# Optimization experiments

Measured on AMD Instinct MI355X. Metric: run time of the kernel, lower is better.

## Reference

```python
import jax, jax.numpy as jnp
import numpy as np

N_HEADS = 32
N_KV_HEADS = 8
HEAD_DIM = 128
DIM = 4096
ROPE_THETA = 500000.0
B, S = 2, 2048


def setup_inputs() -> dict:
    key = jax.random.key(0)
    k1, k2, k3, k4, k5 = jax.random.split(key, 5)
    sd = 0.02
    return {
        "x": jax.random.normal(k1, (B, S, DIM), dtype=jnp.float32),
        "wq": jax.random.normal(k2, (DIM, N_HEADS * HEAD_DIM), dtype=jnp.float32) * sd,
        "wk": jax.random.normal(k3, (DIM, N_KV_HEADS * HEAD_DIM), dtype=jnp.float32) * sd,
        "wv": jax.random.normal(k4, (DIM, N_KV_HEADS * HEAD_DIM), dtype=jnp.float32) * sd,
        "wo": jax.random.normal(k5, (N_HEADS * HEAD_DIM, DIM), dtype=jnp.float32) * sd,
    }


def _rope_freqs(seqlen, head_dim, theta):
    inv = 1.0 / (theta ** (jnp.arange(0, head_dim, 2, dtype=jnp.float32) / head_dim))
    ang = jnp.arange(seqlen, dtype=jnp.float32)[:, None] * inv[None, :]  # [S, hd/2]
    return jnp.cos(ang), jnp.sin(ang)


def _apply_rope(t, cos, sin):
    # t: [B, S, H, hd]; complex multiply on interleaved (even, odd) pairs
    tr = t.reshape(*t.shape[:-1], HEAD_DIM // 2, 2)
    a, b = tr[..., 0], tr[..., 1]
    c = cos[None, :, None, :]
    s = sin[None, :, None, :]
    out = jnp.stack([a * c - b * s, a * s + b * c], axis=-1)
    return out.reshape(t.shape)


def reference(x, wq, wk, wv, wo):
    bsz, seqlen, _ = x.shape
    n_rep = N_HEADS // N_KV_HEADS
    q = (x @ wq).reshape(bsz, seqlen, N_HEADS, HEAD_DIM)
    k = (x @ wk).reshape(bsz, seqlen, N_KV_HEADS, HEAD_DIM)
    v = (x @ wv).reshape(bsz, seqlen, N_KV_HEADS, HEAD_DIM)

    cos, sin = _rope_freqs(seqlen, HEAD_DIM, ROPE_THETA)
    q = _apply_rope(q, cos, sin)
    k = _apply_rope(k, cos, sin)

    # repeat_kv: expand kv heads to n_heads (torch.repeat_interleave dim=2)
    k = jnp.repeat(k, n_rep, axis=2)  # [B, S, H, hd]
    v = jnp.repeat(v, n_rep, axis=2)

    scale = 1.0 / jnp.sqrt(jnp.float32(HEAD_DIM))
    scores = jnp.einsum("bqhd,bkhd->bhqk", q, k) * scale  # [B, H, S, S]
    causal = jnp.tril(jnp.ones((seqlen, seqlen), dtype=bool))
    scores = jnp.where(causal[None, None], scores, jnp.float32(-1e9))
    probs = jax.nn.softmax(scores, axis=-1)
    out = jnp.einsum("bhqk,bkhd->bqhd", probs, v)  # [B, S, H, hd]
    out = out.reshape(bsz, seqlen, N_HEADS * HEAD_DIM)
    return out @ wo
```

## Files before the change

### kernel.cpp

```cpp
#include <hip/hip_runtime.h>
#include <stdint.h>

typedef unsigned short u16;
using short8 = __attribute__((ext_vector_type(8))) short;
using f32x4  = __attribute__((ext_vector_type(4))) float;

#define S_LEN 2048
#define NH 32
#define NKV 8
#define HD 128
#define DIM 4096
#define NQ 4096
#define NKVD 1024

typedef __attribute__((address_space(1))) unsigned int uGLB;
typedef __attribute__((address_space(3))) unsigned int uLDS;

__device__ __forceinline__ void g2l16(const u16* g, u16* l) {
  __builtin_amdgcn_global_load_lds((const uGLB*)g, (uLDS*)l, 16, 0, 0);
}

__device__ __forceinline__ float b2f(u16 u) {
  union { unsigned u32; float f; } x; x.u32 = ((unsigned)u) << 16; return x.f;
}
__device__ __forceinline__ u16 f2b(float f) {
  union { float f; unsigned u32; } x; x.f = f;
  unsigned lsb = (x.u32 >> 16) & 1u;
  x.u32 += 0x7fffu + lsb;
  return (u16)(x.u32 >> 16);
}

__global__ __launch_bounds__(256) void transpose_cast(const float* __restrict__ in,
                                                      u16* __restrict__ out,
                                                      int K, int N) {
  __shared__ float tile[32][33];
  int n0 = blockIdx.x * 32, k0 = blockIdx.y * 32;
  int tx = threadIdx.x, ty = threadIdx.y;
#pragma unroll
  for (int j = 0; j < 4; ++j)
    tile[ty + j * 8][tx] = in[(size_t)(k0 + ty + j * 8) * N + n0 + tx];
  __syncthreads();
#pragma unroll
  for (int j = 0; j < 4; ++j)
    out[(size_t)(n0 + ty + j * 8) * K + k0 + tx] = f2b(tile[tx][ty + j * 8]);
}

__global__ __launch_bounds__(256) void cast_x(const float* __restrict__ in,
                                              u16* __restrict__ out, int n4) {
  int i = blockIdx.x * 256 + threadIdx.x;
  if (i >= n4) return;
  float4 v = reinterpret_cast<const float4*>(in)[i];
  ushort4 u;
  u.x = f2b(v.x); u.y = f2b(v.y); u.z = f2b(v.z); u.w = f2b(v.w);
  reinterpret_cast<ushort4*>(out)[i] = u;
}

__global__ __launch_bounds__(512) void gemm256(const u16* __restrict__ A,
                                               const u16* __restrict__ Bt,
                                               int N,
                                               float* __restrict__ out) {
  const int K = 4096;
  const int NT = 64;
  __shared__ __align__(16) u16 lds[2][2][2][8192];

  int tid  = threadIdx.x;
  int lane = tid & 63, w = tid >> 6;
  int ml   = lane & 15, quad = lane >> 4;
  int wm   = w >> 2, wn = w & 3;

  int bid = blockIdx.y * gridDim.x + blockIdx.x;
  int xcd = bid & 7, idx = bid >> 3;
  int bx = (xcd & 3) * 4 + (idx & 3);
  int by = (xcd >> 2) * 8 + (idx >> 2);
  int m0 = by * 256, n0 = bx * 256;

  int dstB = w * 1024 + lane * 16;
  int r    = dstB >> 7;
  int cg   = ((dstB >> 4) & 7) ^ (r & 7);
  const u16* pA = A  + (size_t)(m0 + r) * K + cg * 8;
  const u16* pB = Bt + (size_t)(n0 + r) * K + cg * 8;

#define STAGE(mat, T, hh) do { \
    int _b = (T) & 1; \
    int _Tc = (T) < NT ? (T) : (NT - 1); \
    const u16* _s = ((mat) ? pB : pA) + (size_t)(hh) * 128 * K + (size_t)_Tc * 64; \
    u16* _d = &lds[_b][mat][hh][w * 512]; \
    g2l16(_s, _d); \
    g2l16(_s + (size_t)64 * K, _d + 4096); \
  } while (0)

  f32x4 acc[8][4] = {};
  int cxa  = (quad ^ (ml & 7)) << 4;
  int aoff = ml * 128 + cxa;
  int boff = (wn & 1) * 8192 + aoff;

  STAGE(0, 0, 0); STAGE(0, 0, 1); STAGE(1, 0, 0); STAGE(1, 0, 1);
  STAGE(0, 1, 0);
  asm volatile("s_waitcnt vmcnt(2)" ::: "memory");
  __builtin_amdgcn_s_barrier();

  short8 af[4][2], bf0[2][2], bf1[2][2];

  for (int t = 0; t < NT; ++t) {
    int buf = t & 1;
    const char* Ab = reinterpret_cast<const char*>(&lds[buf][0][wm][0]);
    const char* Bb = reinterpret_cast<const char*>(&lds[buf][1][wn >> 1][0]);

#pragma unroll
    for (int mi = 0; mi < 4; ++mi)
#pragma unroll
      for (int ks = 0; ks < 2; ++ks)
        af[mi][ks] = *reinterpret_cast<const short8*>(Ab + (aoff ^ (ks << 6)) + mi * 2048);
#pragma unroll
    for (int ni = 0; ni < 2; ++ni)
#pragma unroll
      for (int ks = 0; ks < 2; ++ks)
        bf0[ni][ks] = *reinterpret_cast<const short8*>(Bb + (boff ^ (ks << 6)) + ni * 2048);
    STAGE(0, t + 1, 1);
    __builtin_amdgcn_s_barrier();
    asm volatile("s_waitcnt lgkmcnt(0)" ::: "memory");
    __builtin_amdgcn_sched_barrier(0);
    __builtin_amdgcn_s_setprio(1);
#pragma unroll
    for (int mi = 0; mi < 4; ++mi)
#pragma unroll
      for (int ni = 0; ni < 2; ++ni)
#pragma unroll
        for (int ks = 0; ks < 2; ++ks)
          acc[mi][ni] = __builtin_amdgcn_mfma_f32_16x16x32_bf16(af[mi][ks], bf0[ni][ks], acc[mi][ni], 0, 0, 0);
    __builtin_amdgcn_s_setprio(0);
    __builtin_amdgcn_s_barrier();

#pragma unroll
    for (int ni = 0; ni < 2; ++ni)
#pragma unroll
      for (int ks = 0; ks < 2; ++ks)
        bf1[ni][ks] = *reinterpret_cast<const short8*>(Bb + (boff ^ (ks << 6)) + (2 + ni) * 2048);
    STAGE(1, t + 1, 0);
    __builtin_amdgcn_s_barrier();
    asm volatile("s_waitcnt lgkmcnt(0)" ::: "memory");
    __builtin_amdgcn_sched_barrier(0);
    __builtin_amdgcn_s_setprio(1);
#pragma unroll
    for (int mi = 0; mi < 4; ++mi)
#pragma unroll
      for (int ni = 0; ni < 2; ++ni)
#pragma unroll
        for (int ks = 0; ks < 2; ++ks)
          acc[mi][2 + ni] = __builtin_amdgcn_mfma_f32_16x16x32_bf16(af[mi][ks], bf1[ni][ks], acc[mi][2 + ni], 0, 0, 0);
    __builtin_amdgcn_s_setprio(0);
    __builtin_amdgcn_s_barrier();

#pragma unroll
    for (int mi = 0; mi < 4; ++mi)
#pragma unroll
      for (int ks = 0; ks < 2; ++ks)
        af[mi][ks] = *reinterpret_cast<const short8*>(Ab + 8192 + (aoff ^ (ks << 6)) + mi * 2048);
    STAGE(1, t + 1, 1);
    __builtin_amdgcn_s_barrier();
    asm volatile("s_waitcnt lgkmcnt(0)" ::: "memory");
    __builtin_amdgcn_sched_barrier(0);
    __builtin_amdgcn_s_setprio(1);
#pragma unroll
    for (int mi = 0; mi < 4; ++mi)
#pragma unroll
      for (int ni = 0; ni < 2; ++ni)
#pragma unroll
        for (int ks = 0; ks < 2; ++ks)
          acc[4 + mi][ni] = __builtin_amdgcn_mfma_f32_16x16x32_bf16(af[mi][ks], bf0[ni][ks], acc[4 + mi][ni], 0, 0, 0);
    __builtin_amdgcn_s_setprio(0);
    __builtin_amdgcn_s_barrier();

    STAGE(0, t + 2, 0);
    __builtin_amdgcn_s_barrier();
    __builtin_amdgcn_s_setprio(1);
#pragma unroll
    for (int mi = 0; mi < 4; ++mi)
#pragma unroll
      for (int ni = 0; ni < 2; ++ni)
#pragma unroll
        for (int ks = 0; ks < 2; ++ks)
          acc[4 + mi][2 + ni] = __builtin_amdgcn_mfma_f32_16x16x32_bf16(af[mi][ks], bf1[ni][ks], acc[4 + mi][2 + ni], 0, 0, 0);
    __builtin_amdgcn_s_setprio(0);
    asm volatile("s_waitcnt vmcnt(2)" ::: "memory");
    __builtin_amdgcn_s_barrier();
  }
#undef STAGE

#pragma unroll
  for (int mi = 0; mi < 8; ++mi) {
#pragma unroll
    for (int ni = 0; ni < 4; ++ni) {
#pragma unroll
      for (int rr = 0; rr < 4; ++rr) {
        int row = m0 + wm * 128 + mi * 16 + quad * 4 + rr;
        int col = n0 + wn * 64 + ni * 16 + ml;
        out[(size_t)row * N + col] = acc[mi][ni][rr];
      }
    }
  }
}

__global__ __launch_bounds__(512) void gemm128(const u16* __restrict__ A,
                                               const u16* __restrict__ Bt,
                                               u16* __restrict__ Qb,
                                               u16* __restrict__ Kb,
                                               u16* __restrict__ Vt) {
  const int K = 4096;
  const int NT = 64;
  __shared__ __align__(16) char L[98304];

  int tid  = threadIdx.x;
  int lane = tid & 63, w = tid >> 6;
  int ml   = lane & 15, quad = lane >> 4;
  int wm   = w >> 2, wn = w & 3;

  int bid = blockIdx.y * gridDim.x + blockIdx.x;
  int xcd = bid & 7, idx = bid >> 3;
  int bx = (xcd & 3) * 6 + idx % 6;
  int by = (xcd >> 2) * 16 + idx / 6;
  int m0 = by * 128, n0 = bx * 256;

  int dstB = w * 1024 + lane * 16;
  int r    = dstB >> 7;
  int cg   = ((dstB >> 4) & 7) ^ (r & 7);
  const u16* pA = A  + (size_t)(m0 + r) * K + cg * 8;
  const u16* pB = Bt + (size_t)(n0 + r) * K + cg * 8;

#define STAGE_A(T, h) do { \
    int _b = (T) & 1; int _Tc = (T) < NT ? (T) : (NT - 1); \
    g2l16(pA + (size_t)(h) * 64 * K + (size_t)_Tc * 64, \
          (u16*)(L + _b * 16384 + (h) * 8192 + w * 1024)); \
  } while (0)
#define STAGE_B(T, h) do { \
    int _b = (T) & 1; int _Tc = (T) < NT ? (T) : (NT - 1); \
    const u16* _s = pB + (size_t)(h) * 128 * K + (size_t)_Tc * 64; \
    char* _d = L + 32768 + _b * 32768 + (h) * 16384 + w * 1024; \
    g2l16(_s, (u16*)_d); \
    g2l16(_s + (size_t)64 * K, (u16*)(_d + 8192)); \
  } while (0)

  f32x4 acc[4][4] = {};
  int cxa  = (quad ^ (ml & 7)) << 4;
  int aoff = ml * 128 + cxa;
  int boff = (wn & 1) * 8192 + aoff;

  STAGE_A(0, 0); STAGE_A(0, 1); STAGE_B(0, 0); STAGE_B(0, 1);
  STAGE_B(1, 0); STAGE_B(1, 1);
  asm volatile("s_waitcnt vmcnt(4)" ::: "memory");
  __builtin_amdgcn_s_barrier();

  short8 af[2][2], af2[2][2], bf[4][2];

  for (int t = 0; t < NT; ++t) {
    int buf = t & 1;
    const char* Ab = L + buf * 16384 + wm * 8192;
    const char* Bb = L + 32768 + buf * 32768 + (wn >> 1) * 16384;

#pragma unroll
    for (int mi = 0; mi < 2; ++mi)
#pragma unroll
      for (int ks = 0; ks < 2; ++ks)
        af[mi][ks] = *reinterpret_cast<const short8*>(Ab + (aoff ^ (ks << 6)) + mi * 2048);
#pragma unroll
    for (int ni = 0; ni < 4; ++ni)
#pragma unroll
      for (int ks = 0; ks < 2; ++ks)
        bf[ni][ks] = *reinterpret_cast<const short8*>(Bb + (boff ^ (ks << 6)) + ni * 2048);
    STAGE_A(t + 1, 0); STAGE_A(t + 1, 1);
    __builtin_amdgcn_s_barrier();
    asm volatile("s_waitcnt lgkmcnt(0)" ::: "memory");
    __builtin_amdgcn_sched_barrier(0);
    __builtin_amdgcn_s_setprio(1);
#pragma unroll
    for (int mi = 0; mi < 2; ++mi)
#pragma unroll
      for (int ni = 0; ni < 4; ++ni)
#pragma unroll
        for (int ks = 0; ks < 2; ++ks)
          acc[mi][ni] = __builtin_amdgcn_mfma_f32_16x16x32_bf16(af[mi][ks], bf[ni][ks], acc[mi][ni], 0, 0, 0);
    __builtin_amdgcn_s_setprio(0);
    __builtin_amdgcn_s_barrier();

#pragma unroll
    for (int mi = 0; mi < 2; ++mi)
#pragma unroll
      for (int ks = 0; ks < 2; ++ks)
        af2[mi][ks] = *reinterpret_cast<const short8*>(Ab + 4096 + (aoff ^ (ks << 6)) + mi * 2048);
    STAGE_B(t + 2, 0); STAGE_B(t + 2, 1);
    __builtin_amdgcn_s_barrier();
    asm volatile("s_waitcnt lgkmcnt(0)" ::: "memory");
    __builtin_amdgcn_sched_barrier(0);
    __builtin_amdgcn_s_setprio(1);
#pragma unroll
    for (int mi = 0; mi < 2; ++mi)
#pragma unroll
      for (int ni = 0; ni < 4; ++ni)
#pragma unroll
        for (int ks = 0; ks < 2; ++ks)
          acc[2 + mi][ni] = __builtin_amdgcn_mfma_f32_16x16x32_bf16(af2[mi][ks], bf[ni][ks], acc[2 + mi][ni], 0, 0, 0);
    __builtin_amdgcn_s_setprio(0);
    asm volatile("s_waitcnt vmcnt(4)" ::: "memory");
    __builtin_amdgcn_s_barrier();
  }
#undef STAGE_A
#undef STAGE_B

#pragma unroll
  for (int a = 0; a < 4; ++a) {
#pragma unroll
    for (int ni = 0; ni < 4; ++ni) {
#pragma unroll
      for (int rr = 0; rr < 4; ++rr) {
        int row = m0 + wm * 64 + a * 16 + quad * 4 + rr;
        int col = n0 + wn * 64 + ni * 16 + ml;
        float v = acc[a][ni][rr];
        int b = row >> 11, s = row & (S_LEN - 1);
        if (col < NQ) {
          int h = col >> 7, d = col & 127;
          Qb[((size_t)((b * NH + h) * S_LEN + s)) * HD + d] = f2b(v);
        } else if (col < NQ + NKVD) {
          int cc = col - NQ; int h = cc >> 7, d = cc & 127;
          Kb[((size_t)((b * NKV + h) * S_LEN + s)) * HD + d] = f2b(v);
        } else {
          int cc = col - NQ - NKVD; int h = cc >> 7, d = cc & 127;
          Vt[((size_t)((b * NKV + h) * HD + d)) * S_LEN + s] = f2b(v);
        }
      }
    }
  }
}

__global__ __launch_bounds__(256) void rope_ip(u16* __restrict__ X, int npairs) {
  int idx = blockIdx.x * 256 + threadIdx.x;
  if (idx >= npairs) return;
  int i = idx & 63;
  int s = (idx >> 6) & (S_LEN - 1);
  float inv = __expf(-0.2050369278939421f * (float)i);
  float ang = (float)s * inv;
  float sn, cs;
  sincosf(ang, &sn, &cs);
  ushort2 pr = reinterpret_cast<ushort2*>(X)[idx];
  float a = b2f(pr.x), b = b2f(pr.y);
  ushort2 o;
  o.x = f2b(a * cs - b * sn);
  o.y = f2b(a * sn + b * cs);
  reinterpret_cast<ushort2*>(X)[idx] = o;
}

__global__ __launch_bounds__(256, 3) void flash(const u16* __restrict__ Qb,
                                                const u16* __restrict__ Kb,
                                                const u16* __restrict__ Vt,
                                                u16* __restrict__ AO) {
  __shared__ __align__(16) u16 Ks[64 * 128];
  __shared__ __align__(16) u16 Vs[128 * 64];
  __shared__ __align__(16) u16 Ps[4 * 16 * 80];

  int tid  = threadIdx.x;
  int lane = tid & 63, w = tid >> 6;
  int ml   = lane & 15, quad = lane >> 4;
  int q_tile = blockIdx.x, h = blockIdx.y, b = blockIdx.z;
  int hkv = h >> 2;
  int q0  = q_tile * 64;
  const u16* Qh = Qb + ((size_t)(b * NH + h) * S_LEN) * HD;
  const u16* Kh = Kb + ((size_t)(b * NKV + hkv) * S_LEN) * HD;
  const u16* Vh = Vt + ((size_t)(b * NKV + hkv) * HD) * S_LEN;
  u16* Pw = Ps + w * 16 * 80;

  short8 qf[4];
#pragma unroll
  for (int ks = 0; ks < 4; ++ks)
    qf[ks] = *reinterpret_cast<const short8*>(
        Qh + (size_t)(q0 + w * 16 + ml) * HD + ks * 32 + quad * 8);

  short8 ones8;
  {
    u16 one_b = 0x3f80;
#pragma unroll
    for (int j = 0; j < 8; ++j) ones8[j] = (short)one_b;
  }

  f32x4 o[8] = {};
  f32x4 o9 = {};
  const float SC = 0.12751745f;
  const float BIAS = 18.0f;

  int qg = q0 + w * 16 + ml;
  int ntile = q_tile + 1;
  for (int it = 0; it < ntile; ++it) {
    int kv0 = it * 64;
    __syncthreads();
#pragma unroll
    for (int p = 0; p < 4; ++p) {
      int slot = w * 256 + p * 64 + lane;
      int krow = slot >> 4, kch = slot & 15;
      int ksrc = kch ^ (krow & 15);
      g2l16(Kh + (size_t)(kv0 + krow) * HD + ksrc * 8, &Ks[(w * 256 + p * 64) * 8]);
      int vrow = slot >> 3, vch = slot & 7;
      int vsrc = vch ^ (vrow & 7);
      g2l16(Vh + (size_t)vrow * S_LEN + kv0 + vsrc * 8, &Vs[(w * 256 + p * 64) * 8]);
    }
    __syncthreads();

    f32x4 st[4] = {};
#pragma unroll
    for (int ks = 0; ks < 4; ++ks) {
#pragma unroll
      for (int nt = 0; nt < 4; ++nt) {
        int row = nt * 16 + ml;
        int ch = ((ks << 2) | quad) ^ ml;
        short8 kf = *reinterpret_cast<const short8*>(&Ks[row * 128 + ch * 8]);
        st[nt] = __builtin_amdgcn_mfma_f32_16x16x32_bf16(kf, qf[ks], st[nt], 0, 0, 0);
      }
    }

    bool diag = (it == q_tile);
#pragma unroll
    for (int nt = 0; nt < 4; ++nt) {
      float p0 = exp2f(fmaf(st[nt][0], SC, -BIAS));
      float p1 = exp2f(fmaf(st[nt][1], SC, -BIAS));
      float p2 = exp2f(fmaf(st[nt][2], SC, -BIAS));
      float p3 = exp2f(fmaf(st[nt][3], SC, -BIAS));
      if (diag) {
        int kg = kv0 + nt * 16 + quad * 4;
        if (kg + 0 > qg) p0 = 0.f;
        if (kg + 1 > qg) p1 = 0.f;
        if (kg + 2 > qg) p2 = 0.f;
        if (kg + 3 > qg) p3 = 0.f;
      }
      uint2 pk;
      pk.x = (unsigned)f2b(p0) | ((unsigned)f2b(p1) << 16);
      pk.y = (unsigned)f2b(p2) | ((unsigned)f2b(p3) << 16);
      *reinterpret_cast<uint2*>(&Pw[ml * 80 + nt * 16 + quad * 4]) = pk;
    }

#pragma unroll
    for (int ks2 = 0; ks2 < 2; ++ks2) {
      short8 pf = *reinterpret_cast<const short8*>(&Pw[ml * 80 + ks2 * 32 + quad * 8]);
#pragma unroll
      for (int dt = 0; dt < 8; ++dt) {
        int row = dt * 16 + ml;
        int ch = ((ks2 << 2) | quad) ^ (ml & 7);
        short8 vf = *reinterpret_cast<const short8*>(&Vs[row * 64 + ch * 8]);
        o[dt] = __builtin_amdgcn_mfma_f32_16x16x32_bf16(pf, vf, o[dt], 0, 0, 0);
      }
      o9 = __builtin_amdgcn_mfma_f32_16x16x32_bf16(pf, ones8, o9, 0, 0, 0);
    }
  }

  size_t row_base = (size_t)(b * S_LEN + q0 + w * 16 + quad * 4);
#pragma unroll
  for (int rr = 0; rr < 4; ++rr) {
    float inv_l = 1.0f / o9[rr];
#pragma unroll
    for (int dt = 0; dt < 8; ++dt) {
      int col = h * HD + dt * 16 + ml;
      AO[(row_base + rr) * (size_t)DIM + col] = f2b(o[dt][rr] * inv_l);
    }
  }
}

extern "C" void kernel_launch(void* const* d_in, const int* in_sizes, int n_in,
                              void* d_out, int out_size, void* d_ws, size_t ws_size,
                              hipStream_t stream) {
  const float* x  = (const float*)d_in[0];
  const float* wq = (const float*)d_in[1];
  const float* wk = (const float*)d_in[2];
  const float* wv = (const float*)d_in[3];
  const float* wo = (const float*)d_in[4];
  float* out = (float*)d_out;
  char* ws = (char*)d_ws;

  u16* Wqt = (u16*)(ws + 0);
  u16* Wkt = (u16*)(ws + 33554432);
  u16* Wvt = (u16*)(ws + 41943040);
  u16* Xb  = (u16*)(ws + 50331648);
  u16* Qb  = (u16*)(ws + 83886080);
  u16* Kb  = (u16*)(ws + 117440512);
  u16* Vt  = (u16*)(ws + 125829120);

  transpose_cast<<<dim3(128, 128), dim3(32, 8), 0, stream>>>(wq, Wqt, 4096, 4096);
  transpose_cast<<<dim3(32, 128),  dim3(32, 8), 0, stream>>>(wk, Wkt, 4096, 1024);
  transpose_cast<<<dim3(32, 128),  dim3(32, 8), 0, stream>>>(wv, Wvt, 4096, 1024);
  cast_x<<<16384, 256, 0, stream>>>(x, Xb, 4194304);

  gemm128<<<dim3(24, 32), 512, 0, stream>>>(Xb, Wqt, Qb, Kb, Vt);

  rope_ip<<<32768, 256, 0, stream>>>(Qb, 8388608);
  rope_ip<<<8192, 256, 0, stream>>>(Kb, 2097152);

  transpose_cast<<<dim3(128, 128), dim3(32, 8), 0, stream>>>(wo, Wqt, 4096, 4096);

  flash<<<dim3(32, 32, 2), 256, 0, stream>>>(Qb, Kb, Vt, Xb);

  gemm256<<<dim3(16, 16), 512, 0, stream>>>(Xb, Wqt, 4096, out);
}
```

Before: 806.1 us.

## Double-buffer K/V tiles in flash attention and schedule heavy query tiles first

Double-buffers the K and V LDS tiles so the async global-to-LDS load of the next KV tile is issued before computing on the current one. Explicit vmcnt waits and barriers replace the two __syncthreads per iteration. It also reverses the query-tile order so the longest causal blocks launch first, and pads the P scratch row stride from 80 to 88 to reduce bank conflicts. The doubled LDS footprint lowers the occupancy hint from 3 to 2 blocks per CU, giving up some latency hiding from concurrent blocks.

```diff
diff --git a/kernel.cpp b/kernel.cpp
--- a/kernel.cpp
+++ b/kernel.cpp
@@ -348,24 +348,25 @@
   reinterpret_cast<ushort2*>(X)[idx] = o;
 }
 
-__global__ __launch_bounds__(256, 3) void flash(const u16* __restrict__ Qb,
+__global__ __launch_bounds__(256, 2) void flash(const u16* __restrict__ Qb,
                                                 const u16* __restrict__ Kb,
                                                 const u16* __restrict__ Vt,
                                                 u16* __restrict__ AO) {
-  __shared__ __align__(16) u16 Ks[64 * 128];
-  __shared__ __align__(16) u16 Vs[128 * 64];
-  __shared__ __align__(16) u16 Ps[4 * 16 * 80];
+  __shared__ __align__(16) u16 Ks[2][64 * 128];
+  __shared__ __align__(16) u16 Vs[2][128 * 64];
+  __shared__ __align__(16) u16 Ps[4 * 16 * 88];
 
   int tid  = threadIdx.x;
   int lane = tid & 63, w = tid >> 6;
   int ml   = lane & 15, quad = lane >> 4;
-  int q_tile = blockIdx.x, h = blockIdx.y, b = blockIdx.z;
+  int q_tile = gridDim.x - 1 - blockIdx.x;
+  int h = blockIdx.y, b = blockIdx.z;
   int hkv = h >> 2;
   int q0  = q_tile * 64;
   const u16* Qh = Qb + ((size_t)(b * NH + h) * S_LEN) * HD;
   const u16* Kh = Kb + ((size_t)(b * NKV + hkv) * S_LEN) * HD;
   const u16* Vh = Vt + ((size_t)(b * NKV + hkv) * HD) * S_LEN;
-  u16* Pw = Ps + w * 16 * 80;
+  u16* Pw = Ps + w * 16 * 88;
 
   short8 qf[4];
 #pragma unroll
@@ -385,22 +386,39 @@
   const float SC = 0.12751745f;
   const float BIAS = 18.0f;
 
+#define STAGE_KV(IT, D) do { \
+    int _kv0 = (IT) * 64; \
+    _Pragma("unroll") \
+    for (int p = 0; p < 4; ++p) { \
+      int slot = w * 256 + p * 64 + lane; \
+      int krow = slot >> 4, kch = slot & 15; \
+      int ksrc = kch ^ (krow & 15); \
+      g2l16(Kh + (size_t)(_kv0 + krow) * HD + ksrc * 8, &Ks[D][(w * 256 + p * 64) * 8]); \
+      int vrow = slot >> 3, vch = slot & 7; \
+      int vsrc = vch ^ (vrow & 7); \
+      g2l16(Vh + (size_t)vrow * S_LEN + _kv0 + vsrc * 8, &Vs[D][(w * 256 + p * 64) * 8]); \
+    } \
+  } while (0)
+
   int qg = q0 + w * 16 + ml;
   int ntile = q_tile + 1;
+
+  STAGE_KV(0, 0);
+
   for (int it = 0; it < ntile; ++it) {
+    int cur = it & 1;
+    if (it + 1 < ntile) {
+      STAGE_KV(it + 1, cur ^ 1);
+      asm volatile("s_waitcnt vmcnt(8)" ::: "memory");
+    } else {
+      asm volatile("s_waitcnt vmcnt(0)" ::: "memory");
+    }
+    __builtin_amdgcn_s_barrier();
+    __builtin_amdgcn_sched_barrier(0);
+
     int kv0 = it * 64;
-    __syncthreads();
-#pragma unroll
-    for (int p = 0; p < 4; ++p) {
-      int slot = w * 256 + p * 64 + lane;
-      int krow = slot >> 4, kch = slot & 15;
-      int ksrc = kch ^ (krow & 15);
-      g2l16(Kh + (size_t)(kv0 + krow) * HD + ksrc * 8, &Ks[(w * 256 + p * 64) * 8]);
-      int vrow = slot >> 3, vch = slot & 7;
-      int vsrc = vch ^ (vrow & 7);
-      g2l16(Vh + (size_t)vrow * S_LEN + kv0 + vsrc * 8, &Vs[(w * 256 + p * 64) * 8]);
-    }
-    __syncthreads();
+    const u16* Kc = &Ks[cur][0];
+    const u16* Vc = &Vs[cur][0];
 
     f32x4 st[4] = {};
 #pragma unroll
@@ -409,7 +427,7 @@
       for (int nt = 0; nt < 4; ++nt) {
         int row = nt * 16 + ml;
         int ch = ((ks << 2) | quad) ^ ml;
-        short8 kf = *reinterpret_cast<const short8*>(&Ks[row * 128 + ch * 8]);
+        short8 kf = *reinterpret_cast<const short8*>(&Kc[row * 128 + ch * 8]);
         st[nt] = __builtin_amdgcn_mfma_f32_16x16x32_bf16(kf, qf[ks], st[nt], 0, 0, 0);
       }
     }
@@ -431,22 +449,26 @@
       uint2 pk;
       pk.x = (unsigned)f2b(p0) | ((unsigned)f2b(p1) << 16);
       pk.y = (unsigned)f2b(p2) | ((unsigned)f2b(p3) << 16);
-      *reinterpret_cast<uint2*>(&Pw[ml * 80 + nt * 16 + quad * 4]) = pk;
+      *reinterpret_cast<uint2*>(&Pw[ml * 88 + nt * 16 + quad * 4]) = pk;
     }
 
 #pragma unroll
     for (int ks2 = 0; ks2 < 2; ++ks2) {
-      short8 pf = *reinterpret_cast<const short8*>(&Pw[ml * 80 + ks2 * 32 + quad * 8]);
+      short8 pf = *reinterpret_cast<const short8*>(&Pw[ml * 88 + ks2 * 32 + quad * 8]);
 #pragma unroll
       for (int dt = 0; dt < 8; ++dt) {
         int row = dt * 16 + ml;
         int ch = ((ks2 << 2) | quad) ^ (ml & 7);
-        short8 vf = *reinterpret_cast<const short8*>(&Vs[row * 64 + ch * 8]);
+        short8 vf = *reinterpret_cast<const short8*>(&Vc[row * 64 + ch * 8]);
         o[dt] = __builtin_amdgcn_mfma_f32_16x16x32_bf16(pf, vf, o[dt], 0, 0, 0);
       }
       o9 = __builtin_amdgcn_mfma_f32_16x16x32_bf16(pf, ones8, o9, 0, 0, 0);
     }
-  }
+
+    __builtin_amdgcn_s_barrier();
+    __builtin_amdgcn_sched_barrier(0);
+  }
+#undef STAGE_KV
 
   size_t row_base = (size_t)(b * S_LEN + q0 + w * 16 + quad * 4);
 #pragma unroll
```

After: 800.9 us. No clear change (-0.6%).
